# Kernel tuning notes

Measured on AMD Instinct MI355X. Metric: run time of the kernel, lower is better.

## Reference

```python
import jax, jax.numpy as jnp
import numpy as np

NUM_EMBEDDINGS = 128
EMBEDDING_DIM = 256
COMMITMENT_COST = 0.25
B, T = 64, 2048


def setup_inputs() -> dict:
    key = jax.random.key(0)
    k1, k2 = jax.random.split(key)
    inputs = jax.random.normal(k1, (B, T, EMBEDDING_DIM), dtype=jnp.float32)
    # codebook initialized like nn.Embedding weight (uniform in torch, normal fine for baseline)
    embedding = jax.random.normal(k2, (NUM_EMBEDDINGS, EMBEDDING_DIM), dtype=jnp.float32)
    return {"inputs": inputs, "embedding": embedding}


def reference(inputs, embedding):
    # eval-mode VectorQuantizerEMA.forward
    input_shape = inputs.shape
    flat = inputs.reshape(-1, EMBEDDING_DIM)                      # [N, D]
    distances = (
        jnp.sum(flat * flat, axis=1, keepdims=True)
        + jnp.sum(embedding * embedding, axis=1)
        - 2.0 * jnp.matmul(flat, embedding.T)
    )
    encoding_indices = jnp.argmin(distances, axis=1)              # [N]
    encodings = jax.nn.one_hot(encoding_indices, NUM_EMBEDDINGS, dtype=inputs.dtype)  # [N, K]
    quantized = embedding[encoding_indices].reshape(input_shape)  # gather lookup

    e_latent_loss = jnp.mean((jax.lax.stop_gradient(quantized) - inputs) ** 2)
    loss = COMMITMENT_COST * e_latent_loss

    # straight-through estimator
    quantized_st = inputs + jax.lax.stop_gradient(quantized - inputs)

    avg_probs = jnp.mean(encodings, axis=0)
    perplexity = jnp.exp(-jnp.sum(avg_probs * jnp.log(avg_probs + 1e-10)))

    encoding_indices = encoding_indices.reshape(input_shape[0], input_shape[1])
    return (loss, quantized_st, perplexity, encodings, encoding_indices)
```

## Files before the change

### kernel.cpp

```cpp
#include <hip/hip_runtime.h>
#include <math.h>

#define NUM_K 128
#define DIM   256
#define NROWS (64 * 2048)
#define BLOCK 256

#define RPB   64
#define GRID  (NROWS / RPB)
#define RPB_F 128
#define GRID_F (NROWS / RPB_F)

#define OFF_LOSS 0u
#define OFF_Q    1u
#define OFF_PERP 33554433u
#define OFF_ENC  33554434u
#define OFF_IDX  50331650u

#define WS_EF_FLOATS 512
#define WS_NEEDED    (WS_EF_FLOATS * 4 + 64 * 3 * 64 * 16)

typedef __attribute__((ext_vector_type(8))) short bf16x8;
typedef __attribute__((ext_vector_type(4))) float f32x4;
typedef float f4a __attribute__((ext_vector_type(4), aligned(4)));

union PackU { uint4 u; bf16x8 v; };

__device__ __forceinline__ bf16x8 pack_hi16(const unsigned int* w) {
  PackU p;
  p.u.x = (w[1] & 0xFFFF0000u) | (w[0] >> 16);
  p.u.y = (w[3] & 0xFFFF0000u) | (w[2] >> 16);
  p.u.z = (w[5] & 0xFFFF0000u) | (w[4] >> 16);
  p.u.w = (w[7] & 0xFFFF0000u) | (w[6] >> 16);
  return p.v;
}

__device__ __forceinline__ void split3(const float* xf, bf16x8& a, bf16x8& b, bf16x8& c) {
  unsigned int ua[8], ub[8], uc[8];
  #pragma unroll
  for (int i = 0; i < 8; ++i) {
    float x = xf[i];
    unsigned int ha = __float_as_uint(x) & 0xFFFF0000u;
    float r1 = x - __uint_as_float(ha);
    unsigned int hb = __float_as_uint(r1) & 0xFFFF0000u;
    float r2 = r1 - __uint_as_float(hb);
    ua[i] = ha; ub[i] = hb; uc[i] = __float_as_uint(r2);
  }
  a = pack_hi16(ua); b = pack_hi16(ub); c = pack_hi16(uc);
}

__global__ void vq_init(const float* __restrict__ E, float* __restrict__ ws) {
    int k = blockIdx.x, lane = threadIdx.x;
    float4 v = *(const float4*)(E + (size_t)k * DIM + lane * 4);
    float s = v.x * v.x + v.y * v.y + v.z * v.z + v.w * v.w;
    #pragma unroll
    for (int off = 32; off; off >>= 1) s += __shfl_down(s, off);
    if (lane == 0) ws[256 + k] = s;
    if (k == 0) {
        if (lane == 0) ws[0] = 0.0f;
        ((int*)ws)[64 + lane]  = 0;
        ((int*)ws)[128 + lane] = 0;
    }
}

__global__ void vq_esplit(const float* __restrict__ E, float* __restrict__ ws) {
    int b = blockIdx.x, lane = threadIdx.x;
    int code = (b & 7) * 16 + (lane & 15);
    int d0   = (b >> 3) * 32 + (lane >> 4) * 8;
    const float* p = E + (size_t)code * DIM + d0;
    float4 v0 = *(const float4*)(p);
    float4 v1 = *(const float4*)(p + 4);
    float xf[8] = {v0.x, v0.y, v0.z, v0.w, v1.x, v1.y, v1.z, v1.w};
    bf16x8 a, bq, c;
    split3(xf, a, bq, c);
    bf16x8* dst = (bf16x8*)(ws + WS_EF_FLOATS);
    dst[(b * 3 + 0) * 64 + lane] = a;
    dst[(b * 3 + 1) * 64 + lane] = bq;
    dst[(b * 3 + 2) * 64 + lane] = c;
}

__global__ __launch_bounds__(BLOCK, 3) void vq_main(
        const float* __restrict__ X, const float* __restrict__ E,
        float* ws, float* __restrict__ out) {
    const int tid  = threadIdx.x;
    const int lane = tid & 63;
    const int kg   = __builtin_amdgcn_readfirstlane(tid >> 6);
    const int pr   = kg & 1;
    const int rh   = kg >> 1;
    const int l4   = lane & 15;
    const int g    = lane >> 4;
    const int r0   = blockIdx.x * RPB;

    __shared__ float rd[2][RPB];
    __shared__ int   ri[2][RPB];
    __shared__ int   idxs[RPB];
    __shared__ int   hcnt[NUM_K];
    if (tid < NUM_K) hcnt[tid] = 0;

    const float* xb = X + (size_t)(r0 + rh * 32 + l4) * DIM + g * 8;
    const bf16x8* __restrict__ EF = (const bf16x8*)(ws + WS_EF_FLOATS);

    f32x4 acc[2][4];
    #pragma unroll
    for (int rt = 0; rt < 2; ++rt)
        #pragma unroll
        for (int ct = 0; ct < 4; ++ct) acc[rt][ct] = (f32x4)0.0f;
    float sx = 0.0f;

    float4 a00 = *(const float4*)(xb);
    float4 a01 = *(const float4*)(xb + 4);
    float4 a10 = *(const float4*)(xb + 16 * DIM);
    float4 a11 = *(const float4*)(xb + 16 * DIM + 4);

    #pragma unroll
    for (int ch = 0; ch < 8; ++ch) {
        bf16x8 ef[4][3];
        #pragma unroll
        for (int ct = 0; ct < 4; ++ct) {
            const int CB = (ch * 8 + pr * 4 + ct) * 3;
            #pragma unroll
            for (int s = 0; s < 3; ++s) ef[ct][s] = EF[(CB + s) * 64 + lane];
        }
        float4 c00 = a00, c01 = a01, c10 = a10, c11 = a11;
        if (ch < 7) {
            const float* nx = xb + (ch + 1) * 32;
            a00 = *(const float4*)(nx);
            a01 = *(const float4*)(nx + 4);
            a10 = *(const float4*)(nx + 16 * DIM);
            a11 = *(const float4*)(nx + 16 * DIM + 4);
        }
        float x0[8] = {c00.x, c00.y, c00.z, c00.w, c01.x, c01.y, c01.z, c01.w};
        float x1[8] = {c10.x, c10.y, c10.z, c10.w, c11.x, c11.y, c11.z, c11.w};
        if (pr == 0) {
            #pragma unroll
            for (int i = 0; i < 8; ++i) {
                sx = fmaf(x0[i], x0[i], sx);
                sx = fmaf(x1[i], x1[i], sx);
            }
        }
        bf16x8 xa0, xb0, xc0, xa1, xb1, xc1;
        split3(x0, xa0, xb0, xc0);
        split3(x1, xa1, xb1, xc1);
#define MF(XP0, XP1, ES)                                                      \
        _Pragma("unroll")                                                     \
        for (int ct = 0; ct < 4; ++ct) {                                      \
            acc[0][ct] = __builtin_amdgcn_mfma_f32_16x16x32_bf16(XP0, ef[ct][ES], acc[0][ct], 0, 0, 0); \
            acc[1][ct] = __builtin_amdgcn_mfma_f32_16x16x32_bf16(XP1, ef[ct][ES], acc[1][ct], 0, 0, 0); \
        }
        MF(xa0, xa1, 0)
        MF(xa0, xa1, 1)
        MF(xb0, xb1, 0)
        MF(xa0, xa1, 2)
        MF(xc0, xc1, 0)
        MF(xb0, xb1, 1)
#undef MF
    }

    const float* sep = ws + 256 + pr * 64;
    const float se0 = sep[l4];
    const float se1 = sep[l4 + 16];
    const float se2 = sep[l4 + 32];
    const float se3 = sep[l4 + 48];
    const int   cb  = pr * 64 + l4;

    #pragma unroll
    for (int rt = 0; rt < 2; ++rt) {
        #pragma unroll
        for (int r = 0; r < 4; ++r) {
            float t0 = fmaf(-2.0f, acc[rt][0][r], se0);
            float t1 = fmaf(-2.0f, acc[rt][1][r], se1);
            float t2 = fmaf(-2.0f, acc[rt][2][r], se2);
            float t3 = fmaf(-2.0f, acc[rt][3][r], se3);
            float t = t0; int ci = cb;
            if (t1 < t) { t = t1; ci = cb + 16; }
            if (t2 < t) { t = t2; ci = cb + 32; }
            if (t3 < t) { t = t3; ci = cb + 48; }
            #pragma unroll
            for (int m = 1; m <= 8; m <<= 1) {
                float tv = __shfl_xor(t, m);
                int   cv = __shfl_xor(ci, m);
                if (tv < t || (tv == t && cv < ci)) { t = tv; ci = cv; }
            }
            if (l4 == 0) {
                int rl = rh * 32 + rt * 16 + g * 4 + r;
                rd[pr][rl] = t;
                ri[pr][rl] = ci;
            }
        }
    }

    if (pr == 0) {
        #pragma unroll
        for (int m = 1; m <= 32; m <<= 1) sx += __shfl_xor(sx, m);
        if (lane == 0) atomicAdd(&ws[0], sx);
    }
    __syncthreads();

    if (tid < RPB) {
        float dm = rd[0][tid]; int ix = ri[0][tid];
        float t  = rd[1][tid];
        if (t < dm) { dm = t; ix = ri[1][tid]; }
        idxs[tid] = ix;
        out[OFF_IDX + r0 + tid] = (float)ix;
        atomicAdd(&hcnt[ix], 1);
        float v = dm;
        #pragma unroll
        for (int m = 1; m <= 32; m <<= 1) v += __shfl_xor(v, m);
        if (tid == 0) atomicAdd(&ws[0], v);
    }
    __syncthreads();
    if (tid < NUM_K && hcnt[tid]) atomicAdd((int*)ws + 64 + tid, hcnt[tid]);

    #pragma unroll 4
    for (int it = 0; it < 16; ++it) {
        int r  = it * 4 + (tid >> 6);
        int ix = idxs[r];
        float4 v = *(const float4*)(E + (size_t)ix * DIM + (tid & 63) * 4);
        f4a w = {v.x, v.y, v.z, v.w};
        *(f4a*)(out + OFF_Q + (size_t)(r0 + r) * DIM + (tid & 63) * 4) = w;
    }
    #pragma unroll 4
    for (int it = 0; it < 8; ++it) {
        int s  = it * BLOCK + tid;
        int r  = s >> 5;
        int c4 = (s & 31) * 4;
        int ix = idxs[r];
        f4a e4;
        e4.x = (c4     == ix) ? 1.0f : 0.0f;
        e4.y = (c4 + 1 == ix) ? 1.0f : 0.0f;
        e4.z = (c4 + 2 == ix) ? 1.0f : 0.0f;
        e4.w = (c4 + 3 == ix) ? 1.0f : 0.0f;
        *(f4a*)(out + OFF_ENC + (size_t)(r0 + r) * NUM_K + c4) = e4;
    }
}

__global__ __launch_bounds__(BLOCK, 2) void vq_main_f(
        const float* __restrict__ X, const float* __restrict__ E,
        float* ws, float* __restrict__ out) {
    const int tid  = threadIdx.x;
    const int lane = tid & 63;
    const int kg   = __builtin_amdgcn_readfirstlane(tid >> 6);
    const int l4   = lane & 15;
    const int g    = lane >> 4;
    const int r0   = blockIdx.x * RPB_F;

    __shared__ float rd[4][RPB_F];
    __shared__ int   ri[4][RPB_F];
    __shared__ int   idxs[RPB_F];
    __shared__ int   hcnt[NUM_K];
    if (tid < NUM_K) hcnt[tid] = 0;

    const float* xp = X + (size_t)(r0 + l4) * DIM + g * 8;
    const float* ep = E + (size_t)(kg * 32 + l4) * DIM + g * 8;

    f32x4 acc[8][2];
    #pragma unroll
    for (int rt = 0; rt < 8; ++rt) { acc[rt][0] = (f32x4)0.0f; acc[rt][1] = (f32x4)0.0f; }
    float sx = 0.0f;

    #pragma unroll 1
    for (int half = 0; half < 2; ++half) {
        const int kbase = half * 128;
        bf16x8 ea[2][4], eb[2][4], ec[2][4];
        #pragma unroll
        for (int ct = 0; ct < 2; ++ct) {
            #pragma unroll
            for (int ch = 0; ch < 4; ++ch) {
                const float* p = ep + (size_t)ct * 16 * DIM + kbase + ch * 32;
                float4 v0 = *(const float4*)(p);
                float4 v1 = *(const float4*)(p + 4);
                float xf[8] = {v0.x, v0.y, v0.z, v0.w, v1.x, v1.y, v1.z, v1.w};
                split3(xf, ea[ct][ch], eb[ct][ch], ec[ct][ch]);
            }
        }
        #pragma unroll
        for (int rt = 0; rt < 8; ++rt) {
            #pragma unroll
            for (int ch = 0; ch < 4; ++ch) {
                const float* p = xp + (size_t)rt * 16 * DIM + kbase + ch * 32;
                float4 v0 = *(const float4*)(p);
                float4 v1 = *(const float4*)(p + 4);
                float xf[8] = {v0.x, v0.y, v0.z, v0.w, v1.x, v1.y, v1.z, v1.w};
                if (kg == 0) {
                    #pragma unroll
                    for (int i = 0; i < 8; ++i) sx = fmaf(xf[i], xf[i], sx);
                }
                bf16x8 xa, xb, xc;
                split3(xf, xa, xb, xc);
                acc[rt][0] = __builtin_amdgcn_mfma_f32_16x16x32_bf16(xa, ea[0][ch], acc[rt][0], 0, 0, 0);
                acc[rt][1] = __builtin_amdgcn_mfma_f32_16x16x32_bf16(xa, ea[1][ch], acc[rt][1], 0, 0, 0);
                acc[rt][0] = __builtin_amdgcn_mfma_f32_16x16x32_bf16(xa, eb[0][ch], acc[rt][0], 0, 0, 0);
                acc[rt][1] = __builtin_amdgcn_mfma_f32_16x16x32_bf16(xa, eb[1][ch], acc[rt][1], 0, 0, 0);
                acc[rt][0] = __builtin_amdgcn_mfma_f32_16x16x32_bf16(xb, ea[0][ch], acc[rt][0], 0, 0, 0);
                acc[rt][1] = __builtin_amdgcn_mfma_f32_16x16x32_bf16(xb, ea[1][ch], acc[rt][1], 0, 0, 0);
                acc[rt][0] = __builtin_amdgcn_mfma_f32_16x16x32_bf16(xa, ec[0][ch], acc[rt][0], 0, 0, 0);
                acc[rt][1] = __builtin_amdgcn_mfma_f32_16x16x32_bf16(xa, ec[1][ch], acc[rt][1], 0, 0, 0);
                acc[rt][0] = __builtin_amdgcn_mfma_f32_16x16x32_bf16(xc, ea[0][ch], acc[rt][0], 0, 0, 0);
                acc[rt][1] = __builtin_amdgcn_mfma_f32_16x16x32_bf16(xc, ea[1][ch], acc[rt][1], 0, 0, 0);
                acc[rt][0] = __builtin_amdgcn_mfma_f32_16x16x32_bf16(xb, eb[0][ch], acc[rt][0], 0, 0, 0);
                acc[rt][1] = __builtin_amdgcn_mfma_f32_16x16x32_bf16(xb, eb[1][ch], acc[rt][1], 0, 0, 0);
            }
        }
        __syncthreads();
    }

    const float* sep = ws + 256 + kg * 32;
    const float se0 = sep[l4];
    const float se1 = sep[l4 + 16];
    const int   c0  = kg * 32 + l4;

    #pragma unroll
    for (int rt = 0; rt < 8; ++rt) {
        #pragma unroll
        for (int r = 0; r < 4; ++r) {
            float t0 = fmaf(-2.0f, acc[rt][0][r], se0);
            float t1 = fmaf(-2.0f, acc[rt][1][r], se1);
            float t; int ci;
            if (t1 < t0) { t = t1; ci = c0 + 16; } else { t = t0; ci = c0; }
            #pragma unroll
            for (int m = 1; m <= 8; m <<= 1) {
                float tv = __shfl_xor(t, m);
                int   cv = __shfl_xor(ci, m);
                if (tv < t || (tv == t && cv < ci)) { t = tv; ci = cv; }
            }
            if (l4 == 0) {
                int rl = rt * 16 + g * 4 + r;
                rd[kg][rl] = t;
                ri[kg][rl] = ci;
            }
        }
    }

    if (kg == 0) {
        #pragma unroll
        for (int m = 1; m <= 32; m <<= 1) sx += __shfl_xor(sx, m);
        if (lane == 0) atomicAdd(&ws[0], sx);
    }
    __syncthreads();

    if (tid < RPB_F) {
        float dm = rd[0][tid]; int ix = ri[0][tid];
        #pragma unroll
        for (int gg = 1; gg < 4; ++gg) {
            float t = rd[gg][tid];
            if (t < dm) { dm = t; ix = ri[gg][tid]; }
        }
        idxs[tid] = ix;
        out[OFF_IDX + r0 + tid] = (float)ix;
        atomicAdd(&hcnt[ix], 1);
        float v = dm;
        #pragma unroll
        for (int m = 1; m <= 32; m <<= 1) v += __shfl_xor(v, m);
        if ((tid & 63) == 0) atomicAdd(&ws[0], v);
    }
    __syncthreads();
    if (tid < NUM_K && hcnt[tid]) atomicAdd((int*)ws + 64 + tid, hcnt[tid]);

    #pragma unroll 4
    for (int it = 0; it < 32; ++it) {
        int r  = it * 4 + (tid >> 6);
        int ix = idxs[r];
        float4 v = *(const float4*)(E + (size_t)ix * DIM + (tid & 63) * 4);
        f4a w = {v.x, v.y, v.z, v.w};
        *(f4a*)(out + OFF_Q + (size_t)(r0 + r) * DIM + (tid & 63) * 4) = w;
    }
    #pragma unroll 4
    for (int it = 0; it < 16; ++it) {
        int s  = it * BLOCK + tid;
        int r  = s >> 5;
        int c4 = (s & 31) * 4;
        int ix = idxs[r];
        f4a e4;
        e4.x = (c4     == ix) ? 1.0f : 0.0f;
        e4.y = (c4 + 1 == ix) ? 1.0f : 0.0f;
        e4.z = (c4 + 2 == ix) ? 1.0f : 0.0f;
        e4.w = (c4 + 3 == ix) ? 1.0f : 0.0f;
        *(f4a*)(out + OFF_ENC + (size_t)(r0 + r) * NUM_K + c4) = e4;
    }
}

__global__ void vq_final(const float* __restrict__ ws, float* __restrict__ out) {
    int t = threadIdx.x;
    if (t == 0) out[OFF_LOSS] = 0.25f * (ws[0] / (float)((size_t)NROWS * DIM));
    int c = ((const int*)ws)[64 + t];
    float p = (float)c / (float)NROWS;
    float v = p * logf(p + 1e-10f);
    #pragma unroll
    for (int off = 32; off; off >>= 1) v += __shfl_down(v, off);
    __shared__ float red[2];
    if ((t & 63) == 0) red[t >> 6] = v;
    __syncthreads();
    if (t == 0) out[OFF_PERP] = expf(-(red[0] + red[1]));
}

extern "C" void kernel_launch(void* const* d_in, const int* in_sizes, int n_in,
                              void* d_out, int out_size, void* d_ws, size_t ws_size,
                              hipStream_t stream) {
    const float* X = (const float*)d_in[0];
    const float* E = (const float*)d_in[1];
    float* out = (float*)d_out;
    float* ws  = (float*)d_ws;

    vq_init<<<NUM_K, 64, 0, stream>>>(E, ws);
    if (ws_size >= (size_t)WS_NEEDED) {
        vq_esplit<<<64, 64, 0, stream>>>(E, ws);
        vq_main  <<<GRID, BLOCK, 0, stream>>>(X, E, ws, out);
    } else {
        vq_main_f<<<GRID_F, BLOCK, 0, stream>>>(X, E, ws, out);
    }
    vq_final<<<1, 128, 0, stream>>>(ws, out);
}
```

Measured before the change: 358.8 us.

## Merge prep kernels, use v_perm packing, split-plane codebook layout, raise occupancy

The norm-computation and codebook-split kernels are merged into one prep launch, which removes one kernel launch. The bf16 packing now uses v_perm byte selects instead of mask/shift/or sequences. The split codebook is stored as three separate planes, so the third plane is loaded only after the first MFMA group, lowering peak register pressure. With that, launch bounds go from 3 to 4 blocks per SIMD, and s_setprio brackets the MFMA groups. The MFMA issue order changes as well, which may slightly alter float accumulation order, and the higher occupancy target risks register spills.

```diff
diff --git a/kernel.cpp b/kernel.cpp
--- a/kernel.cpp
+++ b/kernel.cpp
@@ -18,7 +18,7 @@
 #define OFF_IDX  50331650u
 
 #define WS_EF_FLOATS 512
-#define WS_NEEDED    (WS_EF_FLOATS * 4 + 64 * 3 * 64 * 16)
+#define WS_NEEDED    (WS_EF_FLOATS * 4 + 3 * 64 * 64 * 16)
 
 typedef __attribute__((ext_vector_type(8))) short bf16x8;
 typedef __attribute__((ext_vector_type(4))) float f32x4;
@@ -26,27 +26,64 @@
 
 union PackU { uint4 u; bf16x8 v; };
 
-__device__ __forceinline__ bf16x8 pack_hi16(const unsigned int* w) {
-  PackU p;
-  p.u.x = (w[1] & 0xFFFF0000u) | (w[0] >> 16);
-  p.u.y = (w[3] & 0xFFFF0000u) | (w[2] >> 16);
-  p.u.z = (w[5] & 0xFFFF0000u) | (w[4] >> 16);
-  p.u.w = (w[7] & 0xFFFF0000u) | (w[6] >> 16);
-  return p.v;
-}
-
 __device__ __forceinline__ void split3(const float* xf, bf16x8& a, bf16x8& b, bf16x8& c) {
-  unsigned int ua[8], ub[8], uc[8];
+  unsigned int xr[8], r1b[8], r2b[8];
   #pragma unroll
   for (int i = 0; i < 8; ++i) {
     float x = xf[i];
-    unsigned int ha = __float_as_uint(x) & 0xFFFF0000u;
-    float r1 = x - __uint_as_float(ha);
-    unsigned int hb = __float_as_uint(r1) & 0xFFFF0000u;
-    float r2 = r1 - __uint_as_float(hb);
-    ua[i] = ha; ub[i] = hb; uc[i] = __float_as_uint(r2);
+    unsigned int xu = __float_as_uint(x);
+    float af = __uint_as_float(xu & 0xFFFF0000u);
+    float r1 = x - af;
+    unsigned int r1u = __float_as_uint(r1);
+    float bf_ = __uint_as_float(r1u & 0xFFFF0000u);
+    float r2 = r1 - bf_;
+    xr[i] = xu; r1b[i] = r1u; r2b[i] = __float_as_uint(r2);
   }
-  a = pack_hi16(ua); b = pack_hi16(ub); c = pack_hi16(uc);
+  PackU pa, pb, pc;
+  pa.u.x = __builtin_amdgcn_perm(xr[1],  xr[0],  0x07060302u);
+  pa.u.y = __builtin_amdgcn_perm(xr[3],  xr[2],  0x07060302u);
+  pa.u.z = __builtin_amdgcn_perm(xr[5],  xr[4],  0x07060302u);
+  pa.u.w = __builtin_amdgcn_perm(xr[7],  xr[6],  0x07060302u);
+  pb.u.x = __builtin_amdgcn_perm(r1b[1], r1b[0], 0x07060302u);
+  pb.u.y = __builtin_amdgcn_perm(r1b[3], r1b[2], 0x07060302u);
+  pb.u.z = __builtin_amdgcn_perm(r1b[5], r1b[4], 0x07060302u);
+  pb.u.w = __builtin_amdgcn_perm(r1b[7], r1b[6], 0x07060302u);
+  pc.u.x = __builtin_amdgcn_perm(r2b[1], r2b[0], 0x07060302u);
+  pc.u.y = __builtin_amdgcn_perm(r2b[3], r2b[2], 0x07060302u);
+  pc.u.z = __builtin_amdgcn_perm(r2b[5], r2b[4], 0x07060302u);
+  pc.u.w = __builtin_amdgcn_perm(r2b[7], r2b[6], 0x07060302u);
+  a = pa.v; b = pb.v; c = pc.v;
+}
+
+__global__ void vq_prep(const float* __restrict__ E, float* __restrict__ ws) {
+    const int lane = threadIdx.x;
+    if (blockIdx.x < NUM_K) {
+        int k = blockIdx.x;
+        float4 v = *(const float4*)(E + (size_t)k * DIM + lane * 4);
+        float s = v.x * v.x + v.y * v.y + v.z * v.z + v.w * v.w;
+        #pragma unroll
+        for (int off = 32; off; off >>= 1) s += __shfl_down(s, off);
+        if (lane == 0) ws[256 + k] = s;
+        if (k == 0) {
+            if (lane == 0) ws[0] = 0.0f;
+            ((int*)ws)[64 + lane]  = 0;
+            ((int*)ws)[128 + lane] = 0;
+        }
+    } else {
+        int b = blockIdx.x - NUM_K;
+        int code = (b & 7) * 16 + (lane & 15);
+        int d0   = (b >> 3) * 32 + (lane >> 4) * 8;
+        const float* p = E + (size_t)code * DIM + d0;
+        float4 v0 = *(const float4*)(p);
+        float4 v1 = *(const float4*)(p + 4);
+        float xf[8] = {v0.x, v0.y, v0.z, v0.w, v1.x, v1.y, v1.z, v1.w};
+        bf16x8 a, bq, c;
+        split3(xf, a, bq, c);
+        bf16x8* dst = (bf16x8*)(ws + WS_EF_FLOATS);
+        dst[0 * 4096 + b * 64 + lane] = a;
+        dst[1 * 4096 + b * 64 + lane] = bq;
+        dst[2 * 4096 + b * 64 + lane] = c;
+    }
 }
 
 __global__ void vq_init(const float* __restrict__ E, float* __restrict__ ws) {
@@ -63,23 +100,7 @@
     }
 }
 
-__global__ void vq_esplit(const float* __restrict__ E, float* __restrict__ ws) {
-    int b = blockIdx.x, lane = threadIdx.x;
-    int code = (b & 7) * 16 + (lane & 15);
-    int d0   = (b >> 3) * 32 + (lane >> 4) * 8;
-    const float* p = E + (size_t)code * DIM + d0;
-    float4 v0 = *(const float4*)(p);
-    float4 v1 = *(const float4*)(p + 4);
-    float xf[8] = {v0.x, v0.y, v0.z, v0.w, v1.x, v1.y, v1.z, v1.w};
-    bf16x8 a, bq, c;
-    split3(xf, a, bq, c);
-    bf16x8* dst = (bf16x8*)(ws + WS_EF_FLOATS);
-    dst[(b * 3 + 0) * 64 + lane] = a;
-    dst[(b * 3 + 1) * 64 + lane] = bq;
-    dst[(b * 3 + 2) * 64 + lane] = c;
-}
-
-__global__ __launch_bounds__(BLOCK, 3) void vq_main(
+__global__ __launch_bounds__(BLOCK, 4) void vq_main(
         const float* __restrict__ X, const float* __restrict__ E,
         float* ws, float* __restrict__ out) {
     const int tid  = threadIdx.x;
@@ -98,7 +119,7 @@
     if (tid < NUM_K) hcnt[tid] = 0;
 
     const float* xb = X + (size_t)(r0 + rh * 32 + l4) * DIM + g * 8;
-    const bf16x8* __restrict__ EF = (const bf16x8*)(ws + WS_EF_FLOATS);
+    const bf16x8* __restrict__ EFp = (const bf16x8*)(ws + WS_EF_FLOATS);
 
     f32x4 acc[2][4];
     #pragma unroll
@@ -114,13 +135,13 @@
 
     #pragma unroll
     for (int ch = 0; ch < 8; ++ch) {
-        bf16x8 ef[4][3];
-        #pragma unroll
-        for (int ct = 0; ct < 4; ++ct) {
-            const int CB = (ch * 8 + pr * 4 + ct) * 3;
-            #pragma unroll
-            for (int s = 0; s < 3; ++s) ef[ct][s] = EF[(CB + s) * 64 + lane];
-        }
+        const int B0 = (ch * 8 + pr * 4) * 64;
+        bf16x8 ea[4], eb[4], ec[4];
+        #pragma unroll
+        for (int ct = 0; ct < 4; ++ct) ea[ct] = EFp[B0 + ct * 64 + lane];
+        #pragma unroll
+        for (int ct = 0; ct < 4; ++ct) eb[ct] = EFp[4096 + B0 + ct * 64 + lane];
+
         float4 c00 = a00, c01 = a01, c10 = a10, c11 = a11;
         if (ch < 7) {
             const float* nx = xb + (ch + 1) * 32;
@@ -141,18 +162,25 @@
         bf16x8 xa0, xb0, xc0, xa1, xb1, xc1;
         split3(x0, xa0, xb0, xc0);
         split3(x1, xa1, xb1, xc1);
-#define MF(XP0, XP1, ES)                                                      \
+
+#define MF(XP0, XP1, EP)                                                      \
         _Pragma("unroll")                                                     \
         for (int ct = 0; ct < 4; ++ct) {                                      \
-            acc[0][ct] = __builtin_amdgcn_mfma_f32_16x16x32_bf16(XP0, ef[ct][ES], acc[0][ct], 0, 0, 0); \
-            acc[1][ct] = __builtin_amdgcn_mfma_f32_16x16x32_bf16(XP1, ef[ct][ES], acc[1][ct], 0, 0, 0); \
-        }
-        MF(xa0, xa1, 0)
-        MF(xa0, xa1, 1)
-        MF(xb0, xb1, 0)
-        MF(xa0, xa1, 2)
-        MF(xc0, xc1, 0)
-        MF(xb0, xb1, 1)
+            acc[0][ct] = __builtin_amdgcn_mfma_f32_16x16x32_bf16(XP0, EP[ct], acc[0][ct], 0, 0, 0); \
+            acc[1][ct] = __builtin_amdgcn_mfma_f32_16x16x32_bf16(XP1, EP[ct], acc[1][ct], 0, 0, 0); \
+        }
+        __builtin_amdgcn_s_setprio(1);
+        MF(xc0, xc1, ea)
+        MF(xb0, xb1, ea)
+        MF(xa0, xa1, ea)
+        __builtin_amdgcn_s_setprio(0);
+        #pragma unroll
+        for (int ct = 0; ct < 4; ++ct) ec[ct] = EFp[8192 + B0 + ct * 64 + lane];
+        __builtin_amdgcn_s_setprio(1);
+        MF(xb0, xb1, eb)
+        MF(xa0, xa1, eb)
+        MF(xa0, xa1, ec)
+        __builtin_amdgcn_s_setprio(0);
 #undef MF
     }
 
@@ -401,11 +429,11 @@
     float* out = (float*)d_out;
     float* ws  = (float*)d_ws;
 
-    vq_init<<<NUM_K, 64, 0, stream>>>(E, ws);
     if (ws_size >= (size_t)WS_NEEDED) {
-        vq_esplit<<<64, 64, 0, stream>>>(E, ws);
-        vq_main  <<<GRID, BLOCK, 0, stream>>>(X, E, ws, out);
+        vq_prep<<<NUM_K + 64, 64, 0, stream>>>(E, ws);
+        vq_main<<<GRID, BLOCK, 0, stream>>>(X, E, ws, out);
     } else {
+        vq_init<<<NUM_K, 64, 0, stream>>>(E, ws);
         vq_main_f<<<GRID_F, BLOCK, 0, stream>>>(X, E, ws, out);
     }
     vq_final<<<1, 128, 0, stream>>>(ws, out);
```

Result: no change. 361.2 us (+0.6%).
